# Kernel optimization log

Measured on AMD Instinct MI355X. Metric: run time of the kernel, lower is better.

Reference implementation:

```python
import jax, jax.numpy as jnp
import numpy as np

N_HEADS = 16
D_MODEL = 1024
D_K = D_MODEL // N_HEADS
B, T = 2, 2048


def setup_inputs() -> dict:
    key = jax.random.key(0)
    ks = jax.random.split(key, 12)
    s = 1.0 / np.sqrt(D_MODEL)
    inp = {
        "q": jax.random.normal(ks[0], (B, T, D_MODEL), jnp.float32),
        "k": jax.random.normal(ks[1], (B, T, D_MODEL), jnp.float32),
        "v": jax.random.normal(ks[2], (B, T, D_MODEL), jnp.float32),
        # weights stored as [in, out] (torch Linear weight transposed)
        "Wq": jax.random.normal(ks[3], (D_MODEL, D_MODEL), jnp.float32) * s,
        "bq": jax.random.normal(ks[4], (D_MODEL,), jnp.float32) * s,
        "Wk": jax.random.normal(ks[5], (D_MODEL, D_MODEL), jnp.float32) * s,
        "bk": jax.random.normal(ks[6], (D_MODEL,), jnp.float32) * s,
        "Wv": jax.random.normal(ks[7], (D_MODEL, D_MODEL), jnp.float32) * s,
        "bv": jax.random.normal(ks[8], (D_MODEL,), jnp.float32) * s,
        "Wo": jax.random.normal(ks[9], (D_MODEL, D_MODEL), jnp.float32) * s,
        "bo": jax.random.normal(ks[10], (D_MODEL,), jnp.float32) * s,
        "alpha": jnp.ones((1, N_HEADS, 1, 1), jnp.float32) * 10.0,
    }
    return inp


def reference(q, k, v, Wq, bq, Wk, bk, Wv, bv, Wo, bo, alpha):
    Bsz, Tlen, _ = q.shape

    def proj(x, W, b):
        # [B,T,D] -> [B,H,T,d_k]
        y = x @ W + b
        return y.reshape(Bsz, Tlen, N_HEADS, D_K).transpose(0, 2, 1, 3)

    qh = proj(q, Wq, bq)
    kh = proj(k, Wk, bk)
    vh = proj(v, Wv, bv)

    scores = jnp.einsum("bhqd,bhkd->bhqk", qh, kh)  # [B,H,T,T]
    norm_q = jnp.linalg.norm(qh, axis=-1)  # [B,H,T]
    norm_k = jnp.linalg.norm(kh, axis=-1)  # [B,H,T]
    D_udps = (norm_q[..., :, None] + norm_k[..., None, :]) ** 2  # [B,H,T,T]
    D_safe = jnp.where(D_udps == 0.0, jnp.inf, D_udps)
    scores = alpha * 4.0 * scores / D_safe
    attn = jax.nn.softmax(scores, axis=-1)
    out = jnp.einsum("bhqk,bhkd->bhqd", attn, vh)
    out = out.transpose(0, 2, 1, 3).reshape(Bsz, Tlen, D_MODEL)
    return out @ Wo + bo
```

## Files before the change

kernel.cpp:

```cpp
#include <hip/hip_runtime.h>
#include <hip/hip_bf16.h>

#define N_HEADS 16
#define D_MODEL 1024
#define D_K     64
#define B_SZ    2
#define T_LEN   2048
#define M_ROWS  (B_SZ * T_LEN)

typedef __bf16 bf16;
typedef __bf16 bf16x4 __attribute__((ext_vector_type(4)));
typedef __bf16 bf16x8 __attribute__((ext_vector_type(8)));
typedef float  f32x4  __attribute__((ext_vector_type(4)));
typedef unsigned int u32;

__device__ __forceinline__ void gload16(const bf16* g, bf16* l) {
    __builtin_amdgcn_global_load_lds(
        (const __attribute__((address_space(1))) u32*)g,
        (__attribute__((address_space(3))) u32*)l, 16, 0, 0);
}

#define WAIT_VM(N) asm volatile("s_waitcnt vmcnt(" #N ")" ::: "memory")

__global__ void wt_kernel(const float* __restrict__ W0, const float* __restrict__ W1,
                          const float* __restrict__ W2, const float* __restrict__ W3,
                          bf16* __restrict__ T0, bf16* __restrict__ T1,
                          bf16* __restrict__ T2, bf16* __restrict__ T3) {
    __shared__ float tile[32][33];
    const int z = blockIdx.z;
    const float* W = (z == 0) ? W0 : (z == 1) ? W1 : (z == 2) ? W2 : W3;
    bf16* Wt       = (z == 0) ? T0 : (z == 1) ? T1 : (z == 2) ? T2 : T3;
    const int tx = threadIdx.x, ty = threadIdx.y;
    const int x0 = blockIdx.x * 32, y0 = blockIdx.y * 32;
    for (int yy = ty; yy < 32; yy += 8)
        tile[yy][tx] = W[(size_t)(y0 + yy) * D_MODEL + x0 + tx];
    __syncthreads();
    for (int yy = ty; yy < 32; yy += 8)
        Wt[(size_t)(x0 + yy) * D_MODEL + y0 + tx] = (bf16)tile[tx][yy];
}

__global__ void conv3_kernel(const float* __restrict__ q, const float* __restrict__ k,
                             const float* __restrict__ v,
                             bf16* __restrict__ qb, bf16* __restrict__ kb,
                             bf16* __restrict__ vb) {
    const int z = blockIdx.y;
    const float* X = (z == 0) ? q : (z == 1) ? k : v;
    bf16* Y        = (z == 0) ? qb : (z == 1) ? kb : vb;
    const size_t i = ((size_t)blockIdx.x * 256 + threadIdx.x) * 8;
    const float4 v0 = *(const float4*)&X[i];
    const float4 v1 = *(const float4*)&X[i + 4];
    bf16x8 y;
    y[0]=(bf16)v0.x; y[1]=(bf16)v0.y; y[2]=(bf16)v0.z; y[3]=(bf16)v0.w;
    y[4]=(bf16)v1.x; y[5]=(bf16)v1.y; y[6]=(bf16)v1.z; y[7]=(bf16)v1.w;
    *(bf16x8*)&Y[i] = y;
}

__global__ __launch_bounds__(256, 3) void proj_kernel(
    const bf16* __restrict__ qb, const bf16* __restrict__ kb, const bf16* __restrict__ vb,
    const bf16* __restrict__ WtQ, const bf16* __restrict__ WtK, const bf16* __restrict__ WtV,
    const float* __restrict__ bqp, const float* __restrict__ bkp, const float* __restrict__ bvp,
    bf16* __restrict__ qh, bf16* __restrict__ kh, bf16* __restrict__ vt)
{
    __shared__ bf16 As[3][128 * 32];
    __shared__ bf16 Bs[3][128 * 32];

    const int hw      = blockIdx.x;
    const int logical = (hw & 7) * 96 + (hw >> 3);
    const int z       = logical >> 8;
    const int r       = logical & 255;
    const int m0      = (r >> 3) * 128;
    const int n0      = (r & 7) * 128;

    const bf16*  A    = (z == 0) ? qb  : (z == 1) ? kb  : vb;
    const bf16*  Bt   = (z == 0) ? WtQ : (z == 1) ? WtK : WtV;
    const float* bias = (z == 0) ? bqp : (z == 1) ? bkp : bvp;
    bf16* Out         = (z == 0) ? qh  : (z == 1) ? kh  : vt;

    const int tid = threadIdx.x, lane = tid & 63, w = tid >> 6;
    const int wm = w >> 1, wn = w & 1, g = lane >> 4, c = lane & 15;

    const int srow = w * 32 + (lane >> 2);
    const int scol = (lane & 3) * 8;
    const bf16* Ag = A  + (size_t)(m0 + srow) * D_MODEL + scol;
    const bf16* Bg = Bt + (size_t)(n0 + srow) * D_MODEL + scol;

    f32x4 acc[4][4] = {};

#define PSTAGE(buf, kk)                                                         \
    do {                                                                        \
        gload16(Ag + (kk),                  &As[buf][(w * 32) * 32]);           \
        gload16(Ag + 16 * D_MODEL + (kk),   &As[buf][(w * 32 + 16) * 32]);      \
        gload16(Bg + (kk),                  &Bs[buf][(w * 32) * 32]);           \
        gload16(Bg + 16 * D_MODEL + (kk),   &Bs[buf][(w * 32 + 16) * 32]);      \
    } while (0)

    PSTAGE(0, 0);
    PSTAGE(1, 32);
    WAIT_VM(4);
    __builtin_amdgcn_s_barrier();

    int cur = 0;
    for (int t = 0; t < 32; ++t) {
        if (t + 2 < 32) {
            int pre = cur + 2; if (pre >= 3) pre -= 3;
            PSTAGE(pre, (t + 2) * 32);
        }

        bf16x8 a[4], b[4];
        #pragma unroll
        for (int i = 0; i < 4; i++) a[i] = *(const bf16x8*)&As[cur][(wm*64 + i*16 + c) * 32 + g*8];
        #pragma unroll
        for (int j = 0; j < 4; j++) b[j] = *(const bf16x8*)&Bs[cur][(wn*64 + j*16 + c) * 32 + g*8];

        __builtin_amdgcn_s_setprio(1);
        if (z != 2) {
            #pragma unroll
            for (int i = 0; i < 4; i++)
                #pragma unroll
                for (int j = 0; j < 4; j++)
                    acc[i][j] = __builtin_amdgcn_mfma_f32_16x16x32_bf16(a[i], b[j], acc[i][j], 0, 0, 0);
        } else {
            #pragma unroll
            for (int i = 0; i < 4; i++)
                #pragma unroll
                for (int j = 0; j < 4; j++)
                    acc[i][j] = __builtin_amdgcn_mfma_f32_16x16x32_bf16(b[j], a[i], acc[i][j], 0, 0, 0);
        }
        __builtin_amdgcn_s_setprio(0);

        if (t + 2 < 32) { WAIT_VM(4); }
        else            { WAIT_VM(0); }
        __builtin_amdgcn_s_barrier();
        cur = (cur + 1 == 3) ? 0 : cur + 1;
    }
#undef PSTAGE

    #pragma unroll
    for (int i = 0; i < 4; i++)
        #pragma unroll
        for (int j = 0; j < 4; j++)
            #pragma unroll
            for (int r4 = 0; r4 < 4; r4++) {
                if (z != 2) {
                    const int mrow = m0 + wm*64 + i*16 + g*4 + r4;
                    const int ncol = n0 + wn*64 + j*16 + c;
                    const float y = acc[i][j][r4] + bias[ncol];
                    const int b_ = mrow >> 11, t_ = mrow & (T_LEN - 1);
                    const int h_ = ncol >> 6,  d_ = ncol & (D_K - 1);
                    Out[(((size_t)(b_*N_HEADS + h_))*T_LEN + t_)*D_K + d_] = (bf16)y;
                } else {
                    const int nrow = n0 + wn*64 + j*16 + g*4 + r4;
                    const int mcol = m0 + wm*64 + i*16 + c;
                    const float y = acc[i][j][r4] + bias[nrow];
                    const int b_ = mcol >> 11, t_ = mcol & (T_LEN - 1);
                    const int h_ = nrow >> 6,  d_ = nrow & (D_K - 1);
                    Out[(((size_t)(b_*N_HEADS + h_))*D_K + d_)*T_LEN + t_] = (bf16)y;
                }
            }
}

__global__ void norm_kernel(const bf16* __restrict__ qh, const bf16* __restrict__ kh,
                            float* __restrict__ nq, float* __restrict__ nk, int nrows) {
    const bf16* X = blockIdx.y ? kh : qh;
    float* O      = blockIdx.y ? nk : nq;
    const int row  = blockIdx.x * 4 + (threadIdx.x >> 6);
    const int lane = threadIdx.x & 63;
    if (row >= nrows) return;
    float v = (float)X[(size_t)row * D_K + lane];
    float s = v * v;
    #pragma unroll
    for (int m = 1; m < 64; m <<= 1) s += __shfl_xor(s, m, 64);
    if (lane == 0) O[row] = sqrtf(s);
}

#define KVB 64

__global__ __launch_bounds__(512, 4) void attn_kernel(
    const bf16* __restrict__ qh, const bf16* __restrict__ kh, const bf16* __restrict__ vt,
    const float* __restrict__ nq, const float* __restrict__ nk,
    const float* __restrict__ alpha, bf16* __restrict__ ao)
{
    __shared__ bf16 Ks[3][KVB * D_K];
    __shared__ bf16 Vs[3][KVB * D_K];
    __shared__ bf16 plds[8][16][72];

    const int bid     = blockIdx.x;
    const int logical = (bid & 7) * 64 + (bid >> 3);
    const int bh      = logical >> 4;
    const int q0b     = (logical & 15) * 128;

    const int tid  = threadIdx.x;
    const int w    = tid >> 6;
    const int lane = tid & 63;
    const int g    = lane >> 4, c = lane & 15;
    const int myq  = q0b + w * 16 + c;
    const int sw   = (c & 7) << 4;

    const int srow = tid >> 3;
    const int sgb  = (((tid & 7) ^ (srow & 7)) << 4);

    const bf16* Q  = qh + (size_t)bh * T_LEN * D_K;
    const bf16* K  = kh + (size_t)bh * T_LEN * D_K;
    const bf16* V  = vt + (size_t)bh * D_K * T_LEN;
    const float* NK = nk + (size_t)bh * T_LEN;

    const float al   = alpha[bh & (N_HEADS - 1)];
    const float a4   = al * 4.0f * 1.44269504f;
    const float negM = -(al * 1.44269504f) - 1e-4f;

    const bf16x8 bq0 = *(const bf16x8*)&Q[(size_t)myq * D_K + g*8];
    const bf16x8 bq1 = *(const bf16x8*)&Q[(size_t)myq * D_K + 32 + g*8];
    const float nq_own = nq[(size_t)bh * T_LEN + myq];

    bf16x8 ones;
    #pragma unroll
    for (int e = 0; e < 8; e++) ones[e] = (bf16)1.0f;

    f32x4 o[4] = {};
    f32x4 o4  = {};

#define AKSTAGE(buf, kn)                                                                          \
    do {                                                                                          \
        gload16((const bf16*)((const char*)&K[(size_t)((kn) + srow) * D_K] + sgb), &Ks[buf][w * 512]); \
        gload16((const bf16*)((const char*)&V[(size_t)srow * T_LEN + (kn)] + sgb), &Vs[buf][w * 512]); \
    } while (0)

    AKSTAGE(0, 0);
    AKSTAGE(1, KVB);
    WAIT_VM(2);
    __builtin_amdgcn_s_barrier();

    const int NT = T_LEN / KVB;
    int cur = 0;
    for (int t = 0; t < NT; ++t) {
        const int k0 = t * KVB;

        float4 nk4[4];
        #pragma unroll
        for (int cb = 0; cb < 4; cb++) nk4[cb] = *(const float4*)&NK[k0 + cb*16 + g*4];
        __builtin_amdgcn_sched_barrier(0);

        if (t + 2 < NT) {
            int pre = cur + 2; if (pre >= 3) pre -= 3;
            AKSTAGE(pre, k0 + 2*KVB);
        }

        f32x4 S[4];
        __builtin_amdgcn_s_setprio(1);
        #pragma unroll
        for (int cb = 0; cb < 4; cb++) {
            const char* kbase = (const char*)&Ks[cur][(size_t)(cb*16 + c) * D_K];
            const bf16x8 ka = *(const bf16x8*)(kbase + ((g*16) ^ sw));
            const bf16x8 kb = *(const bf16x8*)(kbase + ((64 + g*16) ^ sw));
            f32x4 s = {};
            s = __builtin_amdgcn_mfma_f32_16x16x32_bf16(ka, bq0, s, 0, 0, 0);
            s = __builtin_amdgcn_mfma_f32_16x16x32_bf16(kb, bq1, s, 0, 0, 0);
            S[cb] = s;
        }
        __builtin_amdgcn_s_setprio(0);

        #pragma unroll
        for (int cb = 0; cb < 4; cb++) {
            const float nkr[4] = {nk4[cb].x, nk4[cb].y, nk4[cb].z, nk4[cb].w};
            bf16x4 pk;
            #pragma unroll
            for (int r = 0; r < 4; r++) {
                const float den = nq_own + nkr[r];
                const float rr  = __builtin_amdgcn_rcpf(den);
                const float x   = __builtin_fmaf(a4 * S[cb][r], rr * rr, negM);
                pk[r] = (bf16)__builtin_amdgcn_exp2f(x);
            }
            *(bf16x4*)&plds[w][c][cb*16 + g*4] = pk;
        }

        __builtin_amdgcn_s_setprio(1);
        #pragma unroll
        for (int ks = 0; ks < 2; ks++) {
            const bf16x8 pb = *(const bf16x8*)&plds[w][c][ks*32 + g*8];
            #pragma unroll
            for (int f = 0; f < 4; f++) {
                const char* vbase = (const char*)&Vs[cur][(size_t)(f*16 + c) * D_K];
                const bf16x8 vb = *(const bf16x8*)(vbase + ((ks*64 + g*16) ^ sw));
                o[f] = __builtin_amdgcn_mfma_f32_16x16x32_bf16(vb, pb, o[f], 0, 0, 0);
            }
            o4 = __builtin_amdgcn_mfma_f32_16x16x32_bf16(ones, pb, o4, 0, 0, 0);
        }
        __builtin_amdgcn_s_setprio(0);

        if (t + 2 < NT) { WAIT_VM(2); }
        else            { WAIT_VM(0); }
        __builtin_amdgcn_s_barrier();
        cur = (cur + 1 == 3) ? 0 : cur + 1;
    }
#undef AKSTAGE

    const int b_ = bh >> 4, h_ = bh & 15;
    const float inv = 1.0f / o4[0];
    #pragma unroll
    for (int f = 0; f < 4; f++) {
        bf16x4 w4;
        #pragma unroll
        for (int r = 0; r < 4; r++) w4[r] = (bf16)(o[f][r] * inv);
        *(bf16x4*)&ao[((size_t)(b_*T_LEN + myq))*D_MODEL + h_*D_K + f*16 + g*4] = w4;
    }
}

__global__ __launch_bounds__(256, 4) void gemmo_kernel(
    const bf16* __restrict__ A, const bf16* __restrict__ Bt,
    const float* __restrict__ bias, float* __restrict__ Out)
{
    __shared__ bf16 As[2][64 * 32];
    __shared__ bf16 Bs[2][128 * 32];

    const int hw      = blockIdx.x;
    const int logical = (hw & 7) * 64 + (hw >> 3);
    const int m0      = (logical >> 3) * 64;
    const int n0      = (logical & 7) * 128;

    const int tid = threadIdx.x, lane = tid & 63, w = tid >> 6;
    const int wm = w >> 1, wn = w & 1, g = lane >> 4, c = lane & 15;

    const int arow = w * 16 + (lane >> 2);
    const int brow = w * 32 + (lane >> 2);
    const int scol = (lane & 3) * 8;
    const bf16* Ag = A  + (size_t)(m0 + arow) * D_MODEL + scol;
    const bf16* Bg = Bt + (size_t)(n0 + brow) * D_MODEL + scol;

    f32x4 acc[2][4] = {};

#define OSTAGE(buf, kk)                                                         \
    do {                                                                        \
        gload16(Ag + (kk),                &As[buf][(w * 16) * 32]);             \
        gload16(Bg + (kk),                &Bs[buf][(w * 32) * 32]);             \
        gload16(Bg + 16 * D_MODEL + (kk), &Bs[buf][(w * 32 + 16) * 32]);        \
    } while (0)

    OSTAGE(0, 0);
    __syncthreads();

    int cur = 0;
    for (int t = 0; t < 32; ++t) {
        if (t < 31) OSTAGE(cur ^ 1, (t + 1) * 32);

        bf16x8 a[2], b[4];
        #pragma unroll
        for (int i = 0; i < 2; i++) a[i] = *(const bf16x8*)&As[cur][(wm*32 + i*16 + c) * 32 + g*8];
        #pragma unroll
        for (int j = 0; j < 4; j++) b[j] = *(const bf16x8*)&Bs[cur][(wn*64 + j*16 + c) * 32 + g*8];

        __builtin_amdgcn_s_setprio(1);
        #pragma unroll
        for (int i = 0; i < 2; i++)
            #pragma unroll
            for (int j = 0; j < 4; j++)
                acc[i][j] = __builtin_amdgcn_mfma_f32_16x16x32_bf16(a[i], b[j], acc[i][j], 0, 0, 0);
        __builtin_amdgcn_s_setprio(0);
        __syncthreads();
        cur ^= 1;
    }
#undef OSTAGE

    #pragma unroll
    for (int i = 0; i < 2; i++)
        #pragma unroll
        for (int j = 0; j < 4; j++) {
            const int ncol = n0 + wn*64 + j*16 + c;
            const float bb = bias[ncol];
            #pragma unroll
            for (int r = 0; r < 4; r++) {
                const int mrow = m0 + wm*32 + i*16 + g*4 + r;
                Out[(size_t)mrow * D_MODEL + ncol] = acc[i][j][r] + bb;
            }
        }
}

extern "C" void kernel_launch(void* const* d_in, const int* in_sizes, int n_in,
                              void* d_out, int out_size, void* d_ws, size_t ws_size,
                              hipStream_t stream) {
    const float* q     = (const float*)d_in[0];
    const float* k     = (const float*)d_in[1];
    const float* v     = (const float*)d_in[2];
    const float* Wq    = (const float*)d_in[3];
    const float* bq    = (const float*)d_in[4];
    const float* Wk    = (const float*)d_in[5];
    const float* bk    = (const float*)d_in[6];
    const float* Wv    = (const float*)d_in[7];
    const float* bv    = (const float*)d_in[8];
    const float* Wo    = (const float*)d_in[9];
    const float* bo    = (const float*)d_in[10];
    const float* alpha = (const float*)d_in[11];

    char* ws = (char*)d_ws;
    const size_t WBYTES = (size_t)D_MODEL * D_MODEL * sizeof(bf16);
    const size_t HBYTES = (size_t)B_SZ * N_HEADS * T_LEN * D_K * sizeof(bf16);
    const size_t NBYTES = (size_t)B_SZ * N_HEADS * T_LEN * sizeof(float);
    bf16* WtQ = (bf16*)ws;  ws += WBYTES;
    bf16* WtK = (bf16*)ws;  ws += WBYTES;
    bf16* WtV = (bf16*)ws;  ws += WBYTES;
    bf16* WtO = (bf16*)ws;  ws += WBYTES;
    bf16* qh  = (bf16*)ws;  ws += HBYTES;
    bf16* kh  = (bf16*)ws;  ws += HBYTES;
    bf16* vt  = (bf16*)ws;  ws += HBYTES;
    float* nq = (float*)ws; ws += NBYTES;
    float* nk = (float*)ws; ws += NBYTES;
    bf16* ao  = (bf16*)ws;  ws += HBYTES;
    bf16* qb  = (bf16*)ws;  ws += HBYTES;
    bf16* kb  = (bf16*)ws;  ws += HBYTES;
    bf16* vb  = ao;

    wt_kernel<<<dim3(32, 32, 4), dim3(32, 8), 0, stream>>>(
        Wq, Wk, Wv, Wo, WtQ, WtK, WtV, WtO);

    conv3_kernel<<<dim3(M_ROWS * D_MODEL / 8 / 256, 3), 256, 0, stream>>>(
        q, k, v, qb, kb, vb);

    proj_kernel<<<768, 256, 0, stream>>>(
        qb, kb, vb, WtQ, WtK, WtV, bq, bk, bv, qh, kh, vt);

    const int nrows = B_SZ * N_HEADS * T_LEN;
    norm_kernel<<<dim3(nrows / 4, 2), 256, 0, stream>>>(qh, kh, nq, nk, nrows);

    attn_kernel<<<512, 512, 0, stream>>>(qh, kh, vt, nq, nk, alpha, ao);

    gemmo_kernel<<<512, 256, 0, stream>>>(ao, WtO, bo, (float*)d_out);
}
```

Measured before the change: 170.2 us.

## Fuse q/k row norms into projection epilogue and interleave softmax with PV

Row L2 norms of the projected q and k heads are now computed in the projection GEMM epilogue, reducing across the 16 lanes that share a row and writing the norm directly. This drops the separate norm kernel launch and its re-read of qh/kh from global memory. The norm is now taken from fp32 values before bf16 rounding, which differs slightly from the old path. The attention inner loop is also reordered so the exp/softmax for half the key block is followed by its PV MFMAs, then the other half, letting VALU and MFMA work overlap.

After: 149.5 us. 1.14x faster.

```diff
diff --git a/kernel.cpp b/kernel.cpp
--- a/kernel.cpp
+++ b/kernel.cpp
@@ -59,7 +59,8 @@
     const bf16* __restrict__ qb, const bf16* __restrict__ kb, const bf16* __restrict__ vb,
     const bf16* __restrict__ WtQ, const bf16* __restrict__ WtK, const bf16* __restrict__ WtV,
     const float* __restrict__ bqp, const float* __restrict__ bkp, const float* __restrict__ bvp,
-    bf16* __restrict__ qh, bf16* __restrict__ kh, bf16* __restrict__ vt)
+    bf16* __restrict__ qh, bf16* __restrict__ kh, bf16* __restrict__ vt,
+    float* __restrict__ nq, float* __restrict__ nk)
 {
     __shared__ bf16 As[3][128 * 32];
     __shared__ bf16 Bs[3][128 * 32];
@@ -135,42 +136,45 @@
     }
 #undef PSTAGE
 
-    #pragma unroll
-    for (int i = 0; i < 4; i++)
-        #pragma unroll
-        for (int j = 0; j < 4; j++)
+    if (z != 2) {
+        float* nrm = (z == 0) ? nq : nk;
+        const int h_ = (n0 >> 6) + wn;
+        #pragma unroll
+        for (int i = 0; i < 4; i++)
             #pragma unroll
             for (int r4 = 0; r4 < 4; r4++) {
-                if (z != 2) {
-                    const int mrow = m0 + wm*64 + i*16 + g*4 + r4;
+                const int mrow = m0 + wm*64 + i*16 + g*4 + r4;
+                const int b_ = mrow >> 11, t_ = mrow & (T_LEN - 1);
+                float ss = 0.f;
+                #pragma unroll
+                for (int j = 0; j < 4; j++) {
                     const int ncol = n0 + wn*64 + j*16 + c;
                     const float y = acc[i][j][r4] + bias[ncol];
-                    const int b_ = mrow >> 11, t_ = mrow & (T_LEN - 1);
-                    const int h_ = ncol >> 6,  d_ = ncol & (D_K - 1);
-                    Out[(((size_t)(b_*N_HEADS + h_))*T_LEN + t_)*D_K + d_] = (bf16)y;
-                } else {
+                    Out[(((size_t)(b_*N_HEADS + h_))*T_LEN + t_)*D_K + j*16 + c] = (bf16)y;
+                    ss += y * y;
+                }
+                ss += __shfl_xor(ss, 1, 64);
+                ss += __shfl_xor(ss, 2, 64);
+                ss += __shfl_xor(ss, 4, 64);
+                ss += __shfl_xor(ss, 8, 64);
+                if (c == 0)
+                    nrm[((size_t)(b_*N_HEADS + h_))*T_LEN + t_] = sqrtf(ss);
+            }
+    } else {
+        #pragma unroll
+        for (int i = 0; i < 4; i++)
+            #pragma unroll
+            for (int j = 0; j < 4; j++)
+                #pragma unroll
+                for (int r4 = 0; r4 < 4; r4++) {
                     const int nrow = n0 + wn*64 + j*16 + g*4 + r4;
                     const int mcol = m0 + wm*64 + i*16 + c;
                     const float y = acc[i][j][r4] + bias[nrow];
                     const int b_ = mcol >> 11, t_ = mcol & (T_LEN - 1);
-                    const int h_ = nrow >> 6,  d_ = nrow & (D_K - 1);
-                    Out[(((size_t)(b_*N_HEADS + h_))*D_K + d_)*T_LEN + t_] = (bf16)y;
+                    const int h2 = nrow >> 6,  d_ = nrow & (D_K - 1);
+                    Out[(((size_t)(b_*N_HEADS + h2))*D_K + d_)*T_LEN + t_] = (bf16)y;
                 }
-            }
-}
-
-__global__ void norm_kernel(const bf16* __restrict__ qh, const bf16* __restrict__ kh,
-                            float* __restrict__ nq, float* __restrict__ nk, int nrows) {
-    const bf16* X = blockIdx.y ? kh : qh;
-    float* O      = blockIdx.y ? nk : nq;
-    const int row  = blockIdx.x * 4 + (threadIdx.x >> 6);
-    const int lane = threadIdx.x & 63;
-    if (row >= nrows) return;
-    float v = (float)X[(size_t)row * D_K + lane];
-    float s = v * v;
-    #pragma unroll
-    for (int m = 1; m < 64; m <<= 1) s += __shfl_xor(s, m, 64);
-    if (lane == 0) O[row] = sqrtf(s);
+    }
 }
 
 #define KVB 64
@@ -223,6 +227,41 @@
     do {                                                                                          \
         gload16((const bf16*)((const char*)&K[(size_t)((kn) + srow) * D_K] + sgb), &Ks[buf][w * 512]); \
         gload16((const bf16*)((const char*)&V[(size_t)srow * T_LEN + (kn)] + sgb), &Vs[buf][w * 512]); \
+    } while (0)
+
+#define SM(cb)                                                                  \
+    do {                                                                        \
+        const float nkr0 = nk4[cb].x, nkr1 = nk4[cb].y,                         \
+                    nkr2 = nk4[cb].z, nkr3 = nk4[cb].w;                         \
+        bf16x4 pk;                                                              \
+        float den, rr, x;                                                       \
+        den = nq_own + nkr0; rr = __builtin_amdgcn_rcpf(den);                   \
+        x = __builtin_fmaf(a4 * S[cb][0], rr * rr, negM);                       \
+        pk[0] = (bf16)__builtin_amdgcn_exp2f(x);                                \
+        den = nq_own + nkr1; rr = __builtin_amdgcn_rcpf(den);                   \
+        x = __builtin_fmaf(a4 * S[cb][1], rr * rr, negM);                       \
+        pk[1] = (bf16)__builtin_amdgcn_exp2f(x);                                \
+        den = nq_own + nkr2; rr = __builtin_amdgcn_rcpf(den);                   \
+        x = __builtin_fmaf(a4 * S[cb][2], rr * rr, negM);                       \
+        pk[2] = (bf16)__builtin_amdgcn_exp2f(x);                                \
+        den = nq_own + nkr3; rr = __builtin_amdgcn_rcpf(den);                   \
+        x = __builtin_fmaf(a4 * S[cb][3], rr * rr, negM);                       \
+        pk[3] = (bf16)__builtin_amdgcn_exp2f(x);                                \
+        *(bf16x4*)&plds[w][c][(cb)*16 + g*4] = pk;                              \
+    } while (0)
+
+#define PV(ks)                                                                  \
+    do {                                                                        \
+        const bf16x8 pb = *(const bf16x8*)&plds[w][c][(ks)*32 + g*8];           \
+        __builtin_amdgcn_s_setprio(1);                                          \
+        _Pragma("unroll")                                                       \
+        for (int f = 0; f < 4; f++) {                                           \
+            const char* vbase = (const char*)&Vs[cur][(size_t)(f*16 + c) * D_K];\
+            const bf16x8 vb = *(const bf16x8*)(vbase + (((ks)*64 + g*16) ^ sw));\
+            o[f] = __builtin_amdgcn_mfma_f32_16x16x32_bf16(vb, pb, o[f], 0, 0, 0);\
+        }                                                                       \
+        o4 = __builtin_amdgcn_mfma_f32_16x16x32_bf16(ones, pb, o4, 0, 0, 0);    \
+        __builtin_amdgcn_s_setprio(0);                                          \
     } while (0)
 
     AKSTAGE(0, 0);
@@ -259,33 +298,10 @@
         }
         __builtin_amdgcn_s_setprio(0);
 
-        #pragma unroll
-        for (int cb = 0; cb < 4; cb++) {
-            const float nkr[4] = {nk4[cb].x, nk4[cb].y, nk4[cb].z, nk4[cb].w};
-            bf16x4 pk;
-            #pragma unroll
-            for (int r = 0; r < 4; r++) {
-                const float den = nq_own + nkr[r];
-                const float rr  = __builtin_amdgcn_rcpf(den);
-                const float x   = __builtin_fmaf(a4 * S[cb][r], rr * rr, negM);
-                pk[r] = (bf16)__builtin_amdgcn_exp2f(x);
-            }
-            *(bf16x4*)&plds[w][c][cb*16 + g*4] = pk;
-        }
-
-        __builtin_amdgcn_s_setprio(1);
-        #pragma unroll
-        for (int ks = 0; ks < 2; ks++) {
-            const bf16x8 pb = *(const bf16x8*)&plds[w][c][ks*32 + g*8];
-            #pragma unroll
-            for (int f = 0; f < 4; f++) {
-                const char* vbase = (const char*)&Vs[cur][(size_t)(f*16 + c) * D_K];
-                const bf16x8 vb = *(const bf16x8*)(vbase + ((ks*64 + g*16) ^ sw));
-                o[f] = __builtin_amdgcn_mfma_f32_16x16x32_bf16(vb, pb, o[f], 0, 0, 0);
-            }
-            o4 = __builtin_amdgcn_mfma_f32_16x16x32_bf16(ones, pb, o4, 0, 0, 0);
-        }
-        __builtin_amdgcn_s_setprio(0);
+        SM(0); SM(1);
+        PV(0);
+        SM(2); SM(3);
+        PV(1);
 
         if (t + 2 < NT) { WAIT_VM(2); }
         else            { WAIT_VM(0); }
@@ -293,6 +309,8 @@
         cur = (cur + 1 == 3) ? 0 : cur + 1;
     }
 #undef AKSTAGE
+#undef SM
+#undef PV
 
     const int b_ = bh >> 4, h_ = bh & 15;
     const float inv = 1.0f / o4[0];
@@ -415,10 +433,7 @@
         q, k, v, qb, kb, vb);
 
     proj_kernel<<<768, 256, 0, stream>>>(
-        qb, kb, vb, WtQ, WtK, WtV, bq, bk, bv, qh, kh, vt);
-
-    const int nrows = B_SZ * N_HEADS * T_LEN;
-    norm_kernel<<<dim3(nrows / 4, 2), 256, 0, stream>>>(qh, kh, nq, nk, nrows);
+        qb, kb, vb, WtQ, WtK, WtV, bq, bk, bv, qh, kh, vt, nq, nk);
 
     attn_kernel<<<512, 512, 0, stream>>>(qh, kh, vt, nq, nk, alpha, ao);
 
```
